# Optimization experiments

Measured on AMD Instinct MI355X. Metric: run time of the kernel, lower is better.

## Reference

```python
import jax, jax.numpy as jnp
import numpy as np
import math

D_MODEL = 256
N_HEAD = 1
C_IN = 32
B, L = 8, 2048
FACTOR = 5


def _pos_encoding(L, D):
    pos = jnp.arange(L, dtype=jnp.float32)[:, None]
    div = jnp.exp(jnp.arange(0, D, 2, dtype=jnp.float32) * (-math.log(10000.0) / D))
    pe = jnp.zeros((L, D), dtype=jnp.float32)
    pe = pe.at[:, 0::2].set(jnp.sin(pos * div))
    pe = pe.at[:, 1::2].set(jnp.cos(pos * div))
    return pe


def _layer_norm(x, g, b, eps=1e-5):
    mu = x.mean(-1, keepdims=True)
    var = ((x - mu) ** 2).mean(-1, keepdims=True)
    return (x - mu) / jnp.sqrt(var + eps) * g + b


def setup_inputs():
    key = jax.random.key(0)
    ks = jax.random.split(key, 16)
    D = D_MODEL
    s = 0.02
    p = {}
    p["x"] = jax.random.normal(ks[0], (B, L, C_IN), jnp.float32)
    sample_k = min(FACTOR * math.ceil(math.log(L)), L)  # = 40 for L=2048
    p["sample_idx"] = jax.random.randint(ks[1], (L, sample_k), 0, L)
    p["emb_w"] = jax.random.normal(ks[2], (C_IN, N_HEAD * D)) * s
    p["emb_b"] = jnp.zeros((N_HEAD * D,))
    for i, n in enumerate(["wq", "wk", "wv", "wo"]):
        p[n] = jax.random.normal(ks[3 + i], (D, D)) * s
        p["b" + n[1]] = jnp.zeros((D,))
    p["conv1_w"] = jax.random.normal(ks[7], (D, D)) * s  # Conv1d kernel=1 == linear, d_ff = d_model
    p["conv1_b"] = jnp.zeros((D,))
    p["conv2_w"] = jax.random.normal(ks[8], (D, D)) * s
    p["conv2_b"] = jnp.zeros((D,))
    for n in ["ln1", "ln2", "lnf"]:
        p[n + "_g"] = jnp.ones((D,))
        p[n + "_b"] = jnp.zeros((D,))
    p["gru_wih"] = jax.random.normal(ks[9], (3 * D, D)) * s
    p["gru_whh"] = jax.random.normal(ks[10], (3 * D, D)) * s
    p["gru_bih"] = jnp.zeros((3 * D,))
    p["gru_bhh"] = jnp.zeros((3 * D,))
    p["fc_w"] = jax.random.normal(ks[11], (D, 1)) * s
    p["fc_b"] = jnp.zeros((1,))
    return p


def _forward(x, sample_idx, emb_w, emb_b, wq, bq, wk, bk, wv, bv, wo, bo,
             conv1_w, conv1_b, conv2_w, conv2_b, ln1_g, ln1_b, ln2_g, ln2_b,
             lnf_g, lnf_b, gru_wih, gru_whh, gru_bih, gru_bhh, fc_w, fc_b):
    Bx, Lx, _ = x.shape
    H = N_HEAD
    src = x @ emb_w + emb_b + _pos_encoding(Lx, emb_w.shape[1])  # [B,L,D]
    D = src.shape[-1]
    dk = D // H

    def heads(t, w, b):
        return (t @ w + b).reshape(Bx, Lx, H, dk).transpose(0, 2, 1, 3)  # [B,H,L,dk]

    Q = heads(src, wq, bq)
    K = heads(src, wk, bk)
    V = heads(src, wv, bv)

    # ---- ProbSparse attention (Informer, non-masked) ----
    u = sample_idx.shape[1]                                  # n_top == sample_k here
    K_sample = K[:, :, sample_idx, :]                        # [B,H,L,s,dk]
    QK_s = jnp.einsum("bhld,bhlsd->bhls", Q, K_sample)
    M = QK_s.max(-1) - QK_s.sum(-1) / Lx                     # sparsity measure per query
    _, top = jax.lax.top_k(M, u)                             # [B,H,u]
    Q_red = jnp.take_along_axis(Q, top[..., None], axis=2)   # [B,H,u,dk]
    scores = jnp.einsum("bhud,bhkd->bhuk", Q_red, K) / jnp.sqrt(jnp.float32(dk))
    attn = jax.nn.softmax(scores, axis=-1)
    upd = jnp.einsum("bhuk,bhkd->bhud", attn, V)             # [B,H,u,dk]
    ctx = jnp.broadcast_to(V.mean(axis=2, keepdims=True), Q.shape)  # initial context = mean(V)
    bi = jnp.arange(Bx)[:, None, None]
    hi = jnp.arange(H)[None, :, None]
    ctx = ctx.at[bi, hi, top].set(upd)
    out = ctx.transpose(0, 2, 1, 3).reshape(Bx, Lx, D) @ wo + bo

    # ---- EncoderLayer FFN (Conv1d k=1 -> gelu -> Conv1d k=1), residuals, norms ----
    x1 = _layer_norm(src + out, ln1_g, ln1_b)
    y = jax.nn.gelu(x1 @ conv1_w + conv1_b, approximate=False)
    y = y @ conv2_w + conv2_b
    enc = _layer_norm(_layer_norm(x1 + y, ln2_g, ln2_b), lnf_g, lnf_b)

    # ---- GRU: faithful to source bug: seq-major nn.GRU fed [B,L,D] -> scans over batch dim ----
    def step(h, xt):
        gi = xt @ gru_wih.T + gru_bih
        gh = h @ gru_whh.T + gru_bhh
        ir, iz, inn = jnp.split(gi, 3, axis=-1)
        hr, hz, hn = jnp.split(gh, 3, axis=-1)
        r = jax.nn.sigmoid(ir + hr)
        z = jax.nn.sigmoid(iz + hz)
        n = jnp.tanh(inn + r * hn)
        h = (1.0 - z) * n + z * h
        return h, h

    h0 = jnp.zeros((Lx, enc.shape[-1]), enc.dtype)
    _, gru_out = jax.lax.scan(step, h0, enc)  # [B,L,D]
    return gru_out[:, -1, :] @ fc_w + fc_b    # [B,1]


def reference(x, sample_idx, emb_w, emb_b, wq, bq, wk, bk, wv, bv, wo, bo,
              conv1_w, conv1_b, conv2_w, conv2_b, ln1_g, ln1_b, ln2_g, ln2_b,
              lnf_g, lnf_b, gru_wih, gru_whh, gru_bih, gru_bhh, fc_w, fc_b):
    return _forward(x, sample_idx, emb_w, emb_b, wq, bq, wk, bk, wv, bv, wo, bo,
                    conv1_w, conv1_b, conv2_w, conv2_b, ln1_g, ln1_b, ln2_g, ln2_b,
                    lnf_g, lnf_b, gru_wih, gru_whh, gru_bih, gru_bhh, fc_w, fc_b)
```

## Files before the change

kernel.cpp:

```cpp
#include <hip/hip_runtime.h>
#include <hip/hip_bf16.h>
#include <math.h>

#define BB 8
#define LL 2048
#define CIN 32
#define DD 256
#define UU 40
#define NROW (BB*LL)
#define NSL  (NROW*DD)
#define GB 8

typedef unsigned short u16;
typedef __attribute__((ext_vector_type(8))) short short8;
typedef __attribute__((ext_vector_type(4))) float f32x4;

__device__ __forceinline__ u16 f2bf(float v) {
    unsigned u = __float_as_uint(v);
    unsigned r = (u + 0x7FFF + ((u >> 16) & 1)) >> 16;
    return (u16)r;
}
__device__ __forceinline__ float bf2f(u16 h) {
    return __uint_as_float(((unsigned)h) << 16);
}

template<int CTRL>
__device__ __forceinline__ float dpp_add(float v) {
    int s = __builtin_amdgcn_update_dpp(0, __float_as_int(v), CTRL, 0xf, 0xf, true);
    return v + __int_as_float(s);
}
__device__ __forceinline__ float row16_sum(float v) {
    v = dpp_add<0x118>(v);
    v = dpp_add<0x114>(v);
    v = dpp_add<0x112>(v);
    v = dpp_add<0x111>(v);
    return v;
}
__device__ __forceinline__ float dot4(float4 a, float4 b) {
    return a.x * b.x + a.y * b.y + a.z * b.z + a.w * b.w;
}

__global__ __launch_bounds__(256) void src_kernel(
    const float* __restrict__ x, const float* __restrict__ emb_w,
    const float* __restrict__ emb_b,
    u16* __restrict__ srch, u16* __restrict__ srcl, float* __restrict__ srcrow)
{
    __shared__ float xs[CIN];
    const int orig = blockIdx.x;
    const int b = orig & 7;
    const int l = orig >> 3;
    const int r = (b << 11) | l;
    const int d = threadIdx.x;
    if (d < CIN) xs[d] = x[(size_t)r * CIN + d];
    __syncthreads();
    float acc = emb_b[d];
#pragma unroll 8
    for (int c = 0; c < CIN; ++c) acc += xs[c] * emb_w[c * DD + d];
    const int i = d >> 1;
    const float ang = (float)l * expf((float)(2 * i) * (-9.210340371976184f / 256.0f));
    const float pe = (d & 1) ? cosf(ang) : sinf(ang);
    const float v = acc + pe;
    const u16 h = f2bf(v);
    srch[(size_t)r * DD + d] = h;
    srcl[(size_t)r * DD + d] = f2bf(v - bf2f(h));
    if (l == LL - 1) srcrow[b * DD + d] = v;
}

__global__ __launch_bounds__(256) void splitw_kernel(
    const float* __restrict__ wq, const float* __restrict__ wk,
    const float* __restrict__ wv, u16* __restrict__ whT, u16* __restrict__ wlT)
{
    const int o = blockIdx.x, n = blockIdx.y, k = threadIdx.x;
    const float* W = (o == 0) ? wq : (o == 1) ? wk : wv;
    const float v = W[(size_t)k * DD + n];
    const u16 h = f2bf(v);
    whT[((size_t)o << 16) + n * DD + k] = h;
    wlT[((size_t)o << 16) + n * DD + k] = f2bf(v - bf2f(h));
}

__global__ __launch_bounds__(256) void gemm_qkv_mfma(
    const u16* __restrict__ srch, const u16* __restrict__ srcl,
    const u16* __restrict__ whT, const u16* __restrict__ wlT,
    const float* __restrict__ bq, const float* __restrict__ bk,
    const float* __restrict__ bv,
    float* __restrict__ Qf, float* __restrict__ K, float* __restrict__ V,
    float* __restrict__ qrow)
{
    __shared__ __align__(16) u16 AhS[64][40], AlS[64][40], BhS[64][40], BlS[64][40];
    const int t = threadIdx.x;
    const int bx = blockIdx.x;
    const int mt = (bx & 7) * 32 + (bx >> 3);
    const int bm = mt * 64;
    const int bn = blockIdx.y * 64;
    const int o  = blockIdx.z;
    const u16* wh = whT + ((size_t)o << 16);
    const u16* wl = wlT + ((size_t)o << 16);
    const float* bias = (o == 0) ? bq : (o == 1) ? bk : bv;
    float* C = (o == 0) ? Qf : (o == 1) ? K : V;

    const int srow = t >> 2, sk8 = (t & 3) * 8;
    const int lane = t & 63, w = t >> 6;
    const int frow = lane & 15, kg = (lane >> 4) * 8;

    f32x4 acc[4];
#pragma unroll
    for (int nf = 0; nf < 4; ++nf) acc[nf] = (f32x4){0.f, 0.f, 0.f, 0.f};

    for (int ks = 0; ks < 8; ++ks) {
        const int kb = ks * 32 + sk8;
        *(short8*)&AhS[srow][sk8] = *(const short8*)&srch[(size_t)(bm + srow) * DD + kb];
        *(short8*)&AlS[srow][sk8] = *(const short8*)&srcl[(size_t)(bm + srow) * DD + kb];
        *(short8*)&BhS[srow][sk8] = *(const short8*)&wh[(size_t)(bn + srow) * DD + kb];
        *(short8*)&BlS[srow][sk8] = *(const short8*)&wl[(size_t)(bn + srow) * DD + kb];
        __syncthreads();
        const short8 ah = *(const short8*)&AhS[w * 16 + frow][kg];
        const short8 al = *(const short8*)&AlS[w * 16 + frow][kg];
#pragma unroll
        for (int nf = 0; nf < 4; ++nf) {
            const short8 bh = *(const short8*)&BhS[nf * 16 + frow][kg];
            const short8 bl = *(const short8*)&BlS[nf * 16 + frow][kg];
            acc[nf] = __builtin_amdgcn_mfma_f32_16x16x32_bf16(al, bh, acc[nf], 0, 0, 0);
            acc[nf] = __builtin_amdgcn_mfma_f32_16x16x32_bf16(ah, bl, acc[nf], 0, 0, 0);
            acc[nf] = __builtin_amdgcn_mfma_f32_16x16x32_bf16(ah, bh, acc[nf], 0, 0, 0);
        }
        __syncthreads();
    }
#pragma unroll
    for (int nf = 0; nf < 4; ++nf) {
#pragma unroll
        for (int r = 0; r < 4; ++r) {
            const int row = bm + w * 16 + (lane >> 4) * 4 + r;
            const int col = bn + nf * 16 + (lane & 15);
            const float v = acc[nf][r] + bias[col];
            C[(size_t)row * DD + col] = v;
            if (o == 0 && (row & (LL - 1)) == (LL - 1))
                qrow[(row >> 11) * DD + col] = v;
        }
    }
}

__global__ __launch_bounds__(256) void qks_probe(
    const float* __restrict__ Qf, const float* __restrict__ Kf,
    const int* __restrict__ sidx, float* __restrict__ M)
{
    __shared__ float qk[4][UU];
    const int bid = blockIdx.x;
    const int b = bid & 7;
    const int grp = bid >> 3;
    const int t = threadIdx.x;
    const int wv = t >> 6;
    const int lane = t & 63;
    const int sub = lane >> 4;
    const int j = lane & 15;
    const int l = grp * 4 + wv;
    const size_t r = ((size_t)b << 11) + l;

    const int* si = sidx + (size_t)l * UU;
    const int myidx = si[lane < UU ? lane : 0];

    const float4* q4 = (const float4*)&Qf[r * DD];
    const float4 q0 = q4[j * 4 + 0], q1 = q4[j * 4 + 1],
                 q2 = q4[j * 4 + 2], q3 = q4[j * 4 + 3];
    const float* Kb = Kf + ((size_t)b << 11) * DD;

    int idxs[UU / 4];
#pragma unroll
    for (int i = 0; i < UU / 4; ++i) idxs[i] = __shfl(myidx, i * 4 + sub);

#pragma unroll
    for (int i = 0; i < UU / 4; ++i) {
        const float4* kr = (const float4*)&Kb[(size_t)idxs[i] * DD];
        float d = dot4(q0, kr[j * 4 + 0]) + dot4(q1, kr[j * 4 + 1])
                + dot4(q2, kr[j * 4 + 2]) + dot4(q3, kr[j * 4 + 3]);
        d = row16_sum(d);
        if (j == 15) qk[wv][i * 4 + sub] = d;
    }
    __syncthreads();
    if (t < 4) {
        float mx = -1e30f, sm = 0.0f;
#pragma unroll
        for (int s = 0; s < UU; ++s) { float v = qk[t][s]; mx = fmaxf(mx, v); sm += v; }
        M[((size_t)b << 11) + grp * 4 + t] = mx - sm * (1.0f / (float)LL);
    }
}

__global__ __launch_bounds__(256) void rank_kernel(
    const float* __restrict__ M, int* __restrict__ flag)
{
    __shared__ int redi[256];
    const int b = blockIdx.x, t = threadIdx.x;
    const float* Mb = M + (size_t)b * LL;
    const float ref = Mb[LL - 1];
    int cnt = 0;
    for (int l = t; l < LL; l += 256)
        if (l != LL - 1 && Mb[l] >= ref) cnt++;
    redi[t] = cnt; __syncthreads();
    for (int s = 128; s; s >>= 1) { if (t < s) redi[t] += redi[t + s]; __syncthreads(); }
    if (t == 0) flag[b] = (redi[0] < UU) ? 1 : 0;
}

__global__ __launch_bounds__(256) void ctx_scores(
    const float* __restrict__ qrow, const float* __restrict__ K,
    const int* __restrict__ flag, float* __restrict__ sc)
{
    const int b = blockIdx.x;
    if (!flag[b]) return;
    const int t = threadIdx.x, grp = t >> 4, j = t & 15;
    const size_t base = (size_t)b * LL * DD;
    const float4* qr = (const float4*)&qrow[b * DD];
    const float4 q0 = qr[j * 4 + 0], q1 = qr[j * 4 + 1],
                 q2 = qr[j * 4 + 2], q3 = qr[j * 4 + 3];
    const int k0 = blockIdx.y * 128 + grp * 8;
#pragma unroll
    for (int i = 0; i < 8; ++i) {
        const int k = k0 + i;
        const float4* kr = (const float4*)&K[base + (size_t)k * DD];
        float d = dot4(q0, kr[j * 4 + 0]) + dot4(q1, kr[j * 4 + 1])
                + dot4(q2, kr[j * 4 + 2]) + dot4(q3, kr[j * 4 + 3]);
        d = row16_sum(d);
        if (j == 15) sc[b * LL + k] = d * (1.0f / 16.0f);
    }
}

__global__ __launch_bounds__(256) void ctx_softmax(
    const int* __restrict__ flag, float* __restrict__ sc, float* __restrict__ ssum)
{
    __shared__ float red[256];
    const int b = blockIdx.x;
    if (!flag[b]) return;
    const int t = threadIdx.x;
    float* s = sc + b * LL;
    float lm = -1e30f;
    for (int k = t; k < LL; k += 256) lm = fmaxf(lm, s[k]);
    red[t] = lm; __syncthreads();
    for (int st = 128; st; st >>= 1) { if (t < st) red[t] = fmaxf(red[t], red[t + st]); __syncthreads(); }
    const float mx = red[0]; __syncthreads();
    float ls = 0.0f;
    for (int k = t; k < LL; k += 256) { float e = expf(s[k] - mx); s[k] = e; ls += e; }
    red[t] = ls; __syncthreads();
    for (int st = 128; st; st >>= 1) { if (t < st) red[t] += red[t + st]; __syncthreads(); }
    if (t == 0) ssum[b] = red[0];
}

__global__ __launch_bounds__(256) void ctx_pv(
    const float* __restrict__ V, const float* __restrict__ sc,
    const int* __restrict__ flag, float* __restrict__ part)
{
    const int b = blockIdx.x, slice = blockIdx.y;
    const int d = threadIdx.x;
    const size_t base = (size_t)b * LL * DD;
    const int k0 = slice * 256;
    float acc = 0.0f;
    if (flag[b]) {
#pragma unroll 4
        for (int k = k0; k < k0 + 256; ++k)
            acc += sc[b * LL + k] * V[base + (size_t)k * DD + d];
    } else {
#pragma unroll 4
        for (int k = k0; k < k0 + 256; ++k)
            acc += V[base + (size_t)k * DD + d];
    }
    part[(b * 8 + slice) * DD + d] = acc;
}

__device__ __forceinline__ float block_sum256(float v, float* red) {
    const int t = threadIdx.x;
    __syncthreads();
    red[t] = v; __syncthreads();
    for (int s = 128; s; s >>= 1) { if (t < s) red[t] += red[t + s]; __syncthreads(); }
    return red[0];
}

__global__ __launch_bounds__(256) void tail_kernel(
    const float* __restrict__ srcrow, const float* __restrict__ part,
    const float* __restrict__ ssum, const int* __restrict__ flag,
    const float* __restrict__ wo, const float* __restrict__ bo,
    const float* __restrict__ c1w, const float* __restrict__ c1b,
    const float* __restrict__ c2w, const float* __restrict__ c2b,
    const float* __restrict__ g1, const float* __restrict__ b1,
    const float* __restrict__ g2, const float* __restrict__ b2,
    const float* __restrict__ gf, const float* __restrict__ bf,
    float* __restrict__ enc)
{
    __shared__ float xs[DD];
    __shared__ float red[DD];
    const int b = blockIdx.x, d = threadIdx.x;

    float cv = 0.0f;
#pragma unroll
    for (int i = 0; i < 8; ++i) cv += part[(b * 8 + i) * DD + d];
    cv = flag[b] ? cv / ssum[b] : cv * (1.0f / (float)LL);

    xs[d] = cv; __syncthreads();
    float o = bo[d];
    for (int j = 0; j < DD; ++j) o += xs[j] * wo[j * DD + d];
    const float v = srcrow[b * DD + d] + o;

    float mu = block_sum256(v, red) * (1.0f / DD);
    float dv = v - mu;
    float var = block_sum256(dv * dv, red) * (1.0f / DD);
    const float x1 = dv * rsqrtf(var + 1e-5f) * g1[d] + b1[d];

    __syncthreads(); xs[d] = x1; __syncthreads();
    float a = c1b[d];
    for (int j = 0; j < DD; ++j) a += xs[j] * c1w[j * DD + d];
    a = 0.5f * a * (1.0f + erff(a * 0.70710678118654752f));

    __syncthreads(); xs[d] = a; __syncthreads();
    float y = c2b[d];
    for (int j = 0; j < DD; ++j) y += xs[j] * c2w[j * DD + d];

    float t2 = x1 + y;
    mu = block_sum256(t2, red) * (1.0f / DD);
    dv = t2 - mu;
    var = block_sum256(dv * dv, red) * (1.0f / DD);
    float t3 = dv * rsqrtf(var + 1e-5f) * g2[d] + b2[d];

    mu = block_sum256(t3, red) * (1.0f / DD);
    dv = t3 - mu;
    var = block_sum256(dv * dv, red) * (1.0f / DD);
    enc[b * DD + d] = dv * rsqrtf(var + 1e-5f) * gf[d] + bf[d];
}

__global__ __launch_bounds__(768) void gru_coop_kernel(
    const float* __restrict__ enc, const float* __restrict__ wih,
    const float* __restrict__ whh, const float* __restrict__ bih,
    const float* __restrict__ bhh, const float* __restrict__ fcw,
    const float* __restrict__ fcb,
    unsigned long long* __restrict__ hpub,
    float* __restrict__ out)
{
    __shared__ float whhS[96][257];
    __shared__ float encS[BB][260];
    __shared__ float giS[96][8];
    __shared__ float hS[DD];
    __shared__ float ghS[96];
    __shared__ float red[256];
    const int g = blockIdx.x, t = threadIdx.x;

#pragma unroll
    for (int i = 0; i < 8; ++i) {
        const int f4 = t + 768 * i;
        const int lr = f4 >> 6, c4 = f4 & 63;
        const int R = (lr >> 5) * 256 + g * 32 + (lr & 31);
        const float4 w = *(const float4*)&whh[(size_t)R * DD + c4 * 4];
        whhS[lr][c4 * 4 + 0] = w.x; whhS[lr][c4 * 4 + 1] = w.y;
        whhS[lr][c4 * 4 + 2] = w.z; whhS[lr][c4 * 4 + 3] = w.w;
    }
    for (int e = t; e < BB * DD; e += 768) encS[e >> 8][e & 255] = enc[e];
    if (t < DD) hS[t] = 0.0f;
    __syncthreads();

    {
        const int lr = t >> 3, b = t & 7;
        const int R = (lr >> 5) * 256 + g * 32 + (lr & 31);
        float acc = bih[R];
        const float4* w4 = (const float4*)&wih[(size_t)R * DD];
#pragma unroll 8
        for (int jc = 0; jc < 64; ++jc) {
            const float4 w = w4[jc];
            acc += encS[b][jc * 4 + 0] * w.x + encS[b][jc * 4 + 1] * w.y
                 + encS[b][jc * 4 + 2] * w.z + encS[b][jc * 4 + 3] * w.w;
        }
        giS[lr][b] = acc;
    }
    __syncthreads();

    for (int step = 1; step <= BB; ++step) {
        const int b = step - 1;
        const int lr = t >> 3, s = t & 7;
        float p = 0.0f;
#pragma unroll
        for (int k = 0; k < 32; ++k) {
            const int c = s * 32 + ((k + s * 4) & 31);
            p += whhS[lr][c] * hS[c];
        }
        p = dpp_add<0x114>(p); p = dpp_add<0x112>(p); p = dpp_add<0x111>(p);
        if (s == 7) ghS[lr] = p + bhh[(lr >> 5) * 256 + g * 32 + (lr & 31)];
        __syncthreads();

        if (t < 32) {
            const float r  = 1.0f / (1.0f + expf(-(giS[t][b]      + ghS[t])));
            const float z  = 1.0f / (1.0f + expf(-(giS[32 + t][b] + ghS[32 + t])));
            const float n  = tanhf(giS[64 + t][b] + r * ghS[64 + t]);
            const float hnew = (1.0f - z) * n + z * hS[g * 32 + t];
            const unsigned long long w =
                ((unsigned long long)(unsigned)step << 32) | (unsigned long long)__float_as_uint(hnew);
            __hip_atomic_store(&hpub[g * 32 + t], w, __ATOMIC_RELAXED, __HIP_MEMORY_SCOPE_AGENT);
        }
        __syncthreads();
        if (t < DD) {
            unsigned long long w;
            do {
                w = __hip_atomic_load(&hpub[t], __ATOMIC_RELAXED, __HIP_MEMORY_SCOPE_AGENT);
            } while ((int)(w >> 32) != step);
            hS[t] = __uint_as_float((unsigned)w);
        }
        __syncthreads();

        if (g == 0) {
            if (t < DD) red[t] = hS[t] * fcw[t];
            __syncthreads();
            for (int st2 = 128; st2; st2 >>= 1) { if (t < st2) red[t] += red[t + st2]; __syncthreads(); }
            if (t == 0) out[b] = red[0] + fcb[0];
            __syncthreads();
        }
    }
}

extern "C" void kernel_launch(void* const* d_in, const int* in_sizes, int n_in,
                              void* d_out, int out_size, void* d_ws, size_t ws_size,
                              hipStream_t stream)
{
    const float* x      = (const float*)d_in[0];
    const int*   sidx   = (const int*)  d_in[1];
    const float* emb_w  = (const float*)d_in[2];
    const float* emb_b  = (const float*)d_in[3];
    const float* wq     = (const float*)d_in[4];
    const float* bq     = (const float*)d_in[5];
    const float* wk     = (const float*)d_in[6];
    const float* bk     = (const float*)d_in[7];
    const float* wv     = (const float*)d_in[8];
    const float* bv     = (const float*)d_in[9];
    const float* wo     = (const float*)d_in[10];
    const float* bo     = (const float*)d_in[11];
    const float* c1w    = (const float*)d_in[12];
    const float* c1b    = (const float*)d_in[13];
    const float* c2w    = (const float*)d_in[14];
    const float* c2b    = (const float*)d_in[15];
    const float* ln1g   = (const float*)d_in[16];
    const float* ln1b   = (const float*)d_in[17];
    const float* ln2g   = (const float*)d_in[18];
    const float* ln2b   = (const float*)d_in[19];
    const float* lnfg   = (const float*)d_in[20];
    const float* lnfb   = (const float*)d_in[21];
    const float* wih    = (const float*)d_in[22];
    const float* whh    = (const float*)d_in[23];
    const float* bih    = (const float*)d_in[24];
    const float* bhh    = (const float*)d_in[25];
    const float* fcw    = (const float*)d_in[26];
    const float* fcb    = (const float*)d_in[27];

    float* ws  = (float*)d_ws;
    float* K    = ws;
    float* V    = K + NSL;
    float* Mv   = V + NSL;
    int*   flag = (int*)(Mv + NROW);
    float* sc   = (float*)(flag + 16);
    float* ssum = sc + BB * LL;
    float* part = ssum + 16;
    float* srcrow = part + BB * 8 * DD;
    float* qrow = srcrow + BB * DD;
    float* enc  = qrow + BB * DD;
    unsigned long long* hpub = (unsigned long long*)(enc + BB * DD);
    u16* srch = (u16*)(hpub + 256);
    u16* srcl = srch + NSL;
    u16* whT  = srcl + NSL;
    u16* wlT  = whT + 3 * 65536;
    float* Qf = (float*)(wlT + 3 * 65536);

    hipMemsetAsync(hpub, 0, 256 * sizeof(unsigned long long), stream);

    splitw_kernel<<<dim3(3, 256), 256, 0, stream>>>(wq, wk, wv, whT, wlT);
    src_kernel<<<NROW, 256, 0, stream>>>(x, emb_w, emb_b, srch, srcl, srcrow);
    gemm_qkv_mfma<<<dim3(256, 4, 3), 256, 0, stream>>>(srch, srcl, whT, wlT,
                                                       bq, bk, bv, Qf, K, V, qrow);
    qks_probe<<<NROW / 4, 256, 0, stream>>>(Qf, K, sidx, Mv);
    rank_kernel<<<BB, 256, 0, stream>>>(Mv, flag);
    ctx_scores<<<dim3(BB, 16), 256, 0, stream>>>(qrow, K, flag, sc);
    ctx_softmax<<<BB, 256, 0, stream>>>(flag, sc, ssum);
    ctx_pv<<<dim3(BB, 8), 256, 0, stream>>>(V, sc, flag, part);
    tail_kernel<<<BB, 256, 0, stream>>>(srcrow, part, ssum, flag, wo, bo,
                                        c1w, c1b, c2w, c2b,
                                        ln1g, ln1b, ln2g, ln2b, lnfg, lnfb, enc);
    gru_coop_kernel<<<GB, 768, 0, stream>>>(enc, wih, whh, bih, bhh, fcw, fcb,
                                            hpub, (float*)d_out);
}
```

Baseline: 188.8 us.

## Enlarge QKV GEMM tiles to 128x128 with 2x2 warp layout and register reuse

The QKV split-bf16 MFMA GEMM moves from 64x64 block tiles to 128x128 tiles. Each of the four waves now computes a 64x64 sub-tile (4x4 MFMA fragments) and keeps its B fragments in registers for reuse across four A fragments. This cuts global and LDS traffic per FLOP and the number of blocks, in exchange for more accumulator registers (64 floats per lane) and a smaller grid of 768 blocks, which may lower occupancy.

```diff
diff --git a/kernel.cpp b/kernel.cpp
--- a/kernel.cpp
+++ b/kernel.cpp
@@ -86,55 +86,73 @@
     float* __restrict__ Qf, float* __restrict__ K, float* __restrict__ V,
     float* __restrict__ qrow)
 {
-    __shared__ __align__(16) u16 AhS[64][40], AlS[64][40], BhS[64][40], BlS[64][40];
+    __shared__ __align__(16) u16 AhS[128][40], AlS[128][40],
+                                 BhS[128][40], BlS[128][40];
     const int t = threadIdx.x;
     const int bx = blockIdx.x;
-    const int mt = (bx & 7) * 32 + (bx >> 3);
-    const int bm = mt * 64;
-    const int bn = blockIdx.y * 64;
+    const int mt = (bx & 7) * 16 + (bx >> 3);
+    const int bm = mt * 128;
+    const int bn = blockIdx.y * 128;
     const int o  = blockIdx.z;
     const u16* wh = whT + ((size_t)o << 16);
     const u16* wl = wlT + ((size_t)o << 16);
     const float* bias = (o == 0) ? bq : (o == 1) ? bk : bv;
     float* C = (o == 0) ? Qf : (o == 1) ? K : V;
 
-    const int srow = t >> 2, sk8 = (t & 3) * 8;
     const int lane = t & 63, w = t >> 6;
+    const int wr = (w >> 1) * 64, wc = (w & 1) * 64;
     const int frow = lane & 15, kg = (lane >> 4) * 8;
 
-    f32x4 acc[4];
-#pragma unroll
-    for (int nf = 0; nf < 4; ++nf) acc[nf] = (f32x4){0.f, 0.f, 0.f, 0.f};
+    f32x4 acc[4][4];
+#pragma unroll
+    for (int mf = 0; mf < 4; ++mf)
+#pragma unroll
+        for (int nf = 0; nf < 4; ++nf) acc[mf][nf] = (f32x4){0.f, 0.f, 0.f, 0.f};
 
     for (int ks = 0; ks < 8; ++ks) {
-        const int kb = ks * 32 + sk8;
-        *(short8*)&AhS[srow][sk8] = *(const short8*)&srch[(size_t)(bm + srow) * DD + kb];
-        *(short8*)&AlS[srow][sk8] = *(const short8*)&srcl[(size_t)(bm + srow) * DD + kb];
-        *(short8*)&BhS[srow][sk8] = *(const short8*)&wh[(size_t)(bn + srow) * DD + kb];
-        *(short8*)&BlS[srow][sk8] = *(const short8*)&wl[(size_t)(bn + srow) * DD + kb];
+        const int kb = ks * 32;
+#pragma unroll
+        for (int e0 = 0; e0 < 512; e0 += 256) {
+            const int e = e0 + t;
+            const int row = e >> 2, c8 = (e & 3) * 8;
+            *(short8*)&AhS[row][c8] = *(const short8*)&srch[(size_t)(bm + row) * DD + kb + c8];
+            *(short8*)&AlS[row][c8] = *(const short8*)&srcl[(size_t)(bm + row) * DD + kb + c8];
+            *(short8*)&BhS[row][c8] = *(const short8*)&wh[(size_t)(bn + row) * DD + kb + c8];
+            *(short8*)&BlS[row][c8] = *(const short8*)&wl[(size_t)(bn + row) * DD + kb + c8];
+        }
         __syncthreads();
-        const short8 ah = *(const short8*)&AhS[w * 16 + frow][kg];
-        const short8 al = *(const short8*)&AlS[w * 16 + frow][kg];
+        short8 bhr[4], blr[4];
 #pragma unroll
         for (int nf = 0; nf < 4; ++nf) {
-            const short8 bh = *(const short8*)&BhS[nf * 16 + frow][kg];
-            const short8 bl = *(const short8*)&BlS[nf * 16 + frow][kg];
-            acc[nf] = __builtin_amdgcn_mfma_f32_16x16x32_bf16(al, bh, acc[nf], 0, 0, 0);
-            acc[nf] = __builtin_amdgcn_mfma_f32_16x16x32_bf16(ah, bl, acc[nf], 0, 0, 0);
-            acc[nf] = __builtin_amdgcn_mfma_f32_16x16x32_bf16(ah, bh, acc[nf], 0, 0, 0);
+            bhr[nf] = *(const short8*)&BhS[wc + nf * 16 + frow][kg];
+            blr[nf] = *(const short8*)&BlS[wc + nf * 16 + frow][kg];
+        }
+#pragma unroll
+        for (int mf = 0; mf < 4; ++mf) {
+            const short8 ah = *(const short8*)&AhS[wr + mf * 16 + frow][kg];
+            const short8 al = *(const short8*)&AlS[wr + mf * 16 + frow][kg];
+#pragma unroll
+            for (int nf = 0; nf < 4; ++nf) {
+                acc[mf][nf] = __builtin_amdgcn_mfma_f32_16x16x32_bf16(al, bhr[nf], acc[mf][nf], 0, 0, 0);
+                acc[mf][nf] = __builtin_amdgcn_mfma_f32_16x16x32_bf16(ah, blr[nf], acc[mf][nf], 0, 0, 0);
+                acc[mf][nf] = __builtin_amdgcn_mfma_f32_16x16x32_bf16(ah, bhr[nf], acc[mf][nf], 0, 0, 0);
+            }
         }
         __syncthreads();
     }
 #pragma unroll
-    for (int nf = 0; nf < 4; ++nf) {
-#pragma unroll
-        for (int r = 0; r < 4; ++r) {
-            const int row = bm + w * 16 + (lane >> 4) * 4 + r;
-            const int col = bn + nf * 16 + (lane & 15);
-            const float v = acc[nf][r] + bias[col];
-            C[(size_t)row * DD + col] = v;
-            if (o == 0 && (row & (LL - 1)) == (LL - 1))
-                qrow[(row >> 11) * DD + col] = v;
+    for (int mf = 0; mf < 4; ++mf) {
+#pragma unroll
+        for (int nf = 0; nf < 4; ++nf) {
+#pragma unroll
+            for (int r = 0; r < 4; ++r) {
+                const int row = bm + wr + mf * 16 + (lane >> 4) * 4 + r;
+                const int col = bn + wc + nf * 16 + (lane & 15);
+                const float v = acc[mf][nf][r] + bias[col];
+                C[(size_t)row * DD + col] = v;
+                if (o == 0 && (row & (LL - 1)) == (LL - 1))
+                    qrow[(row >> 11) * DD + col] = v;
+            }
         }
     }
 }
@@ -463,7 +481,7 @@
 
     splitw_kernel<<<dim3(3, 256), 256, 0, stream>>>(wq, wk, wv, whT, wlT);
     src_kernel<<<NROW, 256, 0, stream>>>(x, emb_w, emb_b, srch, srcl, srcrow);
-    gemm_qkv_mfma<<<dim3(256, 4, 3), 256, 0, stream>>>(srch, srcl, whT, wlT,
+    gemm_qkv_mfma<<<dim3(128, 2, 3), 256, 0, stream>>>(srch, srcl, whT, wlT,
                                                        bq, bk, bv, Qf, K, V, qrow);
     qks_probe<<<NROW / 4, 256, 0, stream>>>(Qf, K, sidx, Mv);
     rank_kernel<<<BB, 256, 0, stream>>>(Mv, flag);
```

Result: no change. 186.8 us (-1.0%).
